# Performance work log

Hardware: AMD Instinct MI355X
Metric: run time of the kernel (lower is better)

Reference implementation:

```python
import jax, jax.numpy as jnp
import numpy as np

B, N, D = 4, 2048, 512   # batch, seq, query_dim
H, DH = 8, 64            # heads, dim_head; inner = H*DH = 512
INNER = H * DH


def setup_inputs() -> dict:
    key = jax.random.key(0)
    ks = jax.random.split(key, 5)
    s = 1.0 / np.sqrt(D)
    return {
        "x": jax.random.normal(ks[0], (B, N, D), dtype=jnp.float32),
        "mask": jnp.ones((B, N), dtype=bool),
        "Wq": jax.random.uniform(ks[1], (D, INNER), jnp.float32, -s, s),
        "Wkv": jax.random.uniform(ks[2], (D, 2 * INNER), jnp.float32, -s, s),
        "Wout": jax.random.uniform(ks[3], (INNER, D), jnp.float32, -s, s),
        "bout": jax.random.uniform(ks[4], (D,), jnp.float32, -s, s),
    }


def reference(x, mask, Wq, Wkv, Wout, bout):
    scale = DH ** -0.5
    q = x @ Wq                                   # [B, N, H*DH]
    kv = x @ Wkv                                 # context defaults to x (self-attn)
    k, v = jnp.split(kv, 2, axis=-1)
    # b n (h d) -> b h n d
    q = q.reshape(B, N, H, DH).transpose(0, 2, 1, 3)
    k = k.reshape(B, N, H, DH).transpose(0, 2, 1, 3)
    v = v.reshape(B, N, H, DH).transpose(0, 2, 1, 3)
    sim = jnp.einsum('bhid,bhjd->bhij', q, k) * scale  # [B, H, N, N]
    max_neg = -jnp.finfo(sim.dtype).max
    sim = jnp.where(mask[:, None, None, :], sim, max_neg)
    attn = jax.nn.softmax(sim, axis=-1)
    out = jnp.einsum('bhij,bhjd->bhid', attn, v)       # [B, H, N, DH]
    out = out.transpose(0, 2, 1, 3).reshape(B, N, INNER)
    return out @ Wout + bout                           # drop_path_rate=0 -> Identity
```

## Files before the change

kernel.cpp:

```cpp
#include <hip/hip_runtime.h>
#include <stdint.h>

typedef __bf16 bf16x8 __attribute__((ext_vector_type(8)));
typedef __bf16 bf16x4 __attribute__((ext_vector_type(4)));
typedef float f32x4 __attribute__((ext_vector_type(4)));
typedef float f32x16 __attribute__((ext_vector_type(16)));
typedef unsigned short u16x8 __attribute__((ext_vector_type(8)));
typedef unsigned short u16x4 __attribute__((ext_vector_type(4)));
typedef unsigned int u32x4 __attribute__((ext_vector_type(4)));

#define MFMA16(a, b, c) __builtin_amdgcn_mfma_f32_16x16x32_bf16((a), (b), (c), 0, 0, 0)
#define MFMA32(a, b, c) __builtin_amdgcn_mfma_f32_32x32x16_bf16((a), (b), (c), 0, 0, 0)
#define EXP2(x) __builtin_amdgcn_exp2f(x)

__device__ __forceinline__ unsigned short f2bf(float f) {
    unsigned int u = __builtin_bit_cast(unsigned int, f);
    return (unsigned short)((u + 0x7fffu + ((u >> 16) & 1u)) >> 16);
}

__device__ __forceinline__ unsigned int cvtpk(float lo, float hi) {
    unsigned int r;
    asm("v_cvt_pk_bf16_f32 %0, %1, %2" : "=v"(r) : "v"(lo), "v"(hi));
    return r;
}

__device__ __forceinline__ void pl32swap(unsigned int& a, unsigned int& b) {
    asm volatile("v_permlane32_swap_b32 %0, %1" : "+v"(a), "+v"(b));
}

__device__ __forceinline__ void gl_lds16(const void* g, void* l) {
    __builtin_amdgcn_global_load_lds(
        (const __attribute__((address_space(1))) unsigned int*)g,
        (__attribute__((address_space(3))) unsigned int*)l, 16, 0, 0);
}

#define BTOK   8192
#define DMODEL 512
#define NQKV   1536
#define SEQ    2048
#define NH     8
#define DH     64
#define QSCL   0.18033688011112043f

__global__ __launch_bounds__(256) void prep_kernel(
    const float* __restrict__ x, const float* __restrict__ Wq,
    const float* __restrict__ Wkv, const float* __restrict__ Wout,
    unsigned short* __restrict__ xb, unsigned short* __restrict__ wqkv_t,
    unsigned short* __restrict__ wout_t)
{
    int64_t idx = (int64_t)blockIdx.x * blockDim.x + threadIdx.x;
    const int64_t NXV = (int64_t)BTOK * DMODEL / 8;
    const int64_t NW1 = (int64_t)NQKV * DMODEL;
    const int64_t NW2 = (int64_t)DMODEL * DMODEL;
    if (idx < NXV) {
        const float* s = x + idx * 8;
        u16x8 o8;
#pragma unroll
        for (int j = 0; j < 8; ++j) o8[j] = f2bf(s[j]);
        *(u16x8*)&xb[idx * 8] = o8;
        return;
    }
    idx -= NXV;
    if (idx < NW1) {
        int o = (int)(idx >> 9), i = (int)(idx & 511);
        float v = (o < 512) ? Wq[i * 512 + o] : Wkv[i * 1024 + (o - 512)];
        wqkv_t[idx] = f2bf(v);
        return;
    }
    idx -= NW1;
    if (idx < NW2) {
        int o = (int)(idx >> 9), i = (int)(idx & 511);
        wout_t[idx] = f2bf(Wout[i * 512 + o]);
    }
}

template <int BF16_OUT, int QSCALE>
__global__ __launch_bounds__(256) void gemm_bt(
    const unsigned short* __restrict__ A, const unsigned short* __restrict__ Bt,
    void* __restrict__ Cout, const float* __restrict__ bias,
    int M, int N, int K)
{
    __shared__ __align__(16) unsigned short As[128 * 32];
    __shared__ __align__(16) unsigned short Bs[128 * 32];
    const int tid = threadIdx.x;
    const int lid = tid & 63, w = tid >> 6;
    const int wr = w >> 1, wc = w & 1;
    const int l16 = lid & 15, lg = lid >> 4;
    const int m0 = blockIdx.x * 128, n0 = blockIdx.y * 128;

    f32x4 acc[4][4] = {};

    for (int k0 = 0; k0 < K; k0 += 32) {
#pragma unroll
        for (int s = 0; s < 2; ++s) {
            int chunk = s * 256 + w * 64 + lid;
            int r = chunk >> 2, off = (chunk & 3) * 8;
            gl_lds16(&A[(int64_t)(m0 + r) * K + k0 + off], &As[(s * 256 + w * 64) * 8]);
            gl_lds16(&Bt[(int64_t)(n0 + r) * K + k0 + off], &Bs[(s * 256 + w * 64) * 8]);
        }
        __syncthreads();
        bf16x8 af[4], bfr[4];
#pragma unroll
        for (int i = 0; i < 4; ++i) {
            af[i]  = *(const bf16x8*)&As[(wr * 64 + i * 16 + l16) * 32 + lg * 8];
            bfr[i] = *(const bf16x8*)&Bs[(wc * 64 + i * 16 + l16) * 32 + lg * 8];
        }
#pragma unroll
        for (int i = 0; i < 4; ++i)
#pragma unroll
            for (int j = 0; j < 4; ++j)
                acc[i][j] = MFMA16(af[i], bfr[j], acc[i][j]);
        __syncthreads();
    }

#pragma unroll
    for (int i = 0; i < 4; ++i) {
        int row = m0 + wr * 64 + i * 16 + lg * 4;
#pragma unroll
        for (int j = 0; j < 4; ++j) {
            int col = n0 + wc * 64 + j * 16 + l16;
#pragma unroll
            for (int e = 0; e < 4; ++e) {
                float v = acc[i][j][e];
                if (QSCALE && col < 512) v *= QSCL;
                if (BF16_OUT) {
                    ((unsigned short*)Cout)[(int64_t)(row + e) * N + col] = f2bf(v);
                } else {
                    ((float*)Cout)[(int64_t)(row + e) * N + col] = v + bias[col];
                }
            }
        }
    }
}

__global__ __launch_bounds__(256, 4) void attn_kernel(
    const unsigned short* __restrict__ qkv, unsigned short* __restrict__ attn_out)
{
    __shared__ __align__(16) char smem[32768];

    const int tid = threadIdx.x;
    const int lid = tid & 63, w = tid >> 6;
    const int qg = w & 1, half = w >> 1;
    const int tid128 = tid & 127;
    const int l31 = lid & 31, g = lid >> 5;

    const int bid = blockIdx.y * 32 + blockIdx.x;
    const int nb = (bid & 7) * 128 + (bid >> 3);
    const int bx = nb & 31, bh = nb >> 5;
    const int b = bh >> 3, h = bh & 7;

    const int64_t rowbase = (int64_t)b * SEQ;
    const unsigned short* qp = qkv + rowbase * NQKV + h * DH;
    const unsigned short* kp = qp + 512;
    const unsigned short* vp = qp + 1024;
    const int qrow = bx * 64 + qg * 32 + l31;

    unsigned short* Hb = (unsigned short*)smem + half * 8192;

    int kro[2], kso[2];
#pragma unroll
    for (int s = 0; s < 2; ++s) {
        int chunk = s * 128 + tid128;
        int r = chunk >> 3, cc = chunk & 7;
        int key = (r ^ (r >> 3)) & 7;
        kro[s] = r; kso[s] = (cc ^ key) * 8;
    }
    const int t4 = tid128 >> 4, d4 = tid128 & 15;
    const int c2wb = t4 >> 2;
    const int kvlo = (2 * t4) & 7;
    int dpart[4];
#pragma unroll
    for (int u = 0; u < 4; ++u)
        dpart[u] = (d4 * 4 + u) * 64 + kvlo * 2;

    const int kk = (l31 ^ (l31 >> 3)) & 7;
    const int kd = ((l31 >> 2) ^ l31) & 3;

    bf16x8 qf[4];
#pragma unroll
    for (int ks = 0; ks < 4; ++ks)
        qf[ks] = *(const bf16x8*)&qp[(int64_t)qrow * NQKV + ks * 16 + g * 8];

    f32x16 ot0 = {}, ot1 = {};
    float ssum = 0.f;
    u16x4 pv[4];

#define STAGE_K(T, BUF) {                                                     \
    const unsigned short* kpt_ = kp + (int64_t)(T) * 32 * NQKV;               \
    unsigned short* kb_ = Hb + (BUF) * 2048;                                  \
    _Pragma("unroll")                                                         \
    for (int s_ = 0; s_ < 2; ++s_)                                            \
        gl_lds16(&kpt_[(int64_t)kro[s_] * NQKV + kso[s_]],                    \
                 &kb_[s_ * 1024 + qg * 512]); }

#define LOAD_V(T) {                                                           \
    const unsigned short* vpt_ = vp + (int64_t)(T) * 32 * NQKV;               \
    _Pragma("unroll")                                                         \
    for (int s_ = 0; s_ < 2; ++s_) {                                          \
        int row_ = s_ * 16 + 2 * t4;                                          \
        pv[s_ * 2]     = *(const u16x4*)&vpt_[(int64_t)row_ * NQKV + d4 * 4];         \
        pv[s_ * 2 + 1] = *(const u16x4*)&vpt_[(int64_t)(row_ + 1) * NQKV + d4 * 4]; } }

#define WRITE_V(BUF) {                                                        \
    char* vb_ = (char*)(Hb + 4096 + (BUF) * 2048);                            \
    _Pragma("unroll")                                                         \
    for (int s_ = 0; s_ < 2; ++s_) {                                          \
        int c2w_ = 2 * s_ + c2wb;                                             \
        _Pragma("unroll")                                                     \
        for (int u_ = 0; u_ < 4; ++u_) {                                      \
            int kdw_ = (d4 & 3) ^ u_;                                         \
            int off_ = dpart[u_] + (((c2w_ ^ kdw_) & 3) * 16);                \
            *(unsigned int*)(vb_ + off_) =                                    \
                (unsigned int)pv[s_ * 2][u_] |                                \
                ((unsigned int)pv[s_ * 2 + 1][u_] << 16);                     \
        } } }

    const int tb = half * 32;
    LOAD_V(tb + 0);
    WRITE_V(0);
    LOAD_V(tb + 1);
    WRITE_V(1);
    STAGE_K(tb + 0, 0);
    __syncthreads();

    const int NT = 32;
    for (int t = 0; t < NT; ++t) {
        const int bc = t & 1, bn = bc ^ 1;
        const bool p1 = (t + 1 < NT), p2 = (t + 2 < NT);

        if (p1) STAGE_K(tb + t + 1, bn);
        if (p2) LOAD_V(tb + t + 2);

        f32x16 st = {};
        {
            const unsigned short* kb = Hb + bc * 2048;
            __builtin_amdgcn_s_setprio(1);
#pragma unroll
            for (int ks = 0; ks < 4; ++ks) {
                int c8 = (ks * 2 + g) ^ kk;
                bf16x8 ka = *(const bf16x8*)&kb[l31 * 64 + c8 * 8];
                st = MFMA32(ka, qf[ks], st);
            }
            __builtin_amdgcn_s_setprio(0);
        }

#pragma unroll
        for (int r = 0; r < 16; ++r) st[r] = EXP2(st[r]);
        float p0 = (st[0] + st[1]) + (st[2] + st[3]);
        float p1v = (st[4] + st[5]) + (st[6] + st[7]);
        float p2v = (st[8] + st[9]) + (st[10] + st[11]);
        float p3v = (st[12] + st[13]) + (st[14] + st[15]);
        ssum += (p0 + p1v) + (p2v + p3v);

        bf16x8 pf[2];
#define PFRAG(HALFI, OUT) {                                               \
        unsigned int a0 = cvtpk(st[8 * HALFI + 0], st[8 * HALFI + 1]);    \
        unsigned int a1 = cvtpk(st[8 * HALFI + 2], st[8 * HALFI + 3]);    \
        unsigned int b0 = cvtpk(st[8 * HALFI + 4], st[8 * HALFI + 5]);    \
        unsigned int b1 = cvtpk(st[8 * HALFI + 6], st[8 * HALFI + 7]);    \
        pl32swap(a0, b0); pl32swap(a1, b1);                               \
        u32x4 t_ = {a0, a1, b0, b1};                                      \
        OUT = __builtin_bit_cast(bf16x8, t_); }
        PFRAG(0, pf[0]); PFRAG(1, pf[1]);
#undef PFRAG

        {
            const unsigned short* vb = Hb + 4096 + bc * 2048;
            __builtin_amdgcn_s_setprio(1);
#pragma unroll
            for (int kstep = 0; kstep < 2; ++kstep) {
                int c2 = (kstep * 2 + g) ^ kd;
                bf16x8 va0 = *(const bf16x8*)&vb[l31 * 32 + c2 * 8];
                bf16x8 va1 = *(const bf16x8*)&vb[(32 + l31) * 32 + c2 * 8];
                ot0 = MFMA32(va0, pf[kstep], ot0);
                ot1 = MFMA32(va1, pf[kstep], ot1);
            }
            __builtin_amdgcn_s_setprio(0);
        }

        if (p1) __syncthreads();
        if (p2) WRITE_V(bc);
    }
#undef STAGE_K
#undef LOAD_V
#undef WRITE_V

    ssum += __shfl_xor(ssum, 32);

    __syncthreads();
    float* Ob  = (float*)smem;
    float* Ssb = (float*)(smem + 16896);
    if (half) {
        float* dst = Ob + (qg * 64 + lid) * 33;
#pragma unroll
        for (int r = 0; r < 16; ++r) { dst[r] = ot0[r]; dst[16 + r] = ot1[r]; }
        Ssb[qg * 64 + lid] = ssum;
    }
    __syncthreads();
    if (!half) {
        const float* src = Ob + (qg * 64 + lid) * 33;
        float inv = 1.0f / (ssum + Ssb[qg * 64 + lid]);
        unsigned short* op = attn_out + (rowbase + qrow) * 512 + h * DH;
#pragma unroll
        for (int rr = 0; rr < 4; ++rr) {
            int d0 = 8 * rr + 4 * g;
            bf16x4 o0, o1;
#pragma unroll
            for (int e = 0; e < 4; ++e) {
                o0[e] = (__bf16)((ot0[rr * 4 + e] + src[rr * 4 + e]) * inv);
                o1[e] = (__bf16)((ot1[rr * 4 + e] + src[16 + rr * 4 + e]) * inv);
            }
            *(bf16x4*)&op[d0] = o0;
            *(bf16x4*)&op[32 + d0] = o1;
        }
    }
}

extern "C" void kernel_launch(void* const* d_in, const int* in_sizes, int n_in,
                              void* d_out, int out_size, void* d_ws, size_t ws_size,
                              hipStream_t stream)
{
    const float* x    = (const float*)d_in[0];
    const float* Wq   = (const float*)d_in[2];
    const float* Wkv  = (const float*)d_in[3];
    const float* Wout = (const float*)d_in[4];
    const float* bout = (const float*)d_in[5];
    float* out = (float*)d_out;

    char* ws = (char*)d_ws;
    unsigned short* xb     = (unsigned short*)(ws);
    unsigned short* wqkv_t = (unsigned short*)(ws + 8388608);
    unsigned short* wout_t = (unsigned short*)(ws + 8388608 + 1572864);
    unsigned short* qkvb   = (unsigned short*)(ws + 10485760);
    unsigned short* attn_o = (unsigned short*)(ws + 35651584);

    prep_kernel<<<6144, 256, 0, stream>>>(x, Wq, Wkv, Wout, xb, wqkv_t, wout_t);

    dim3 g1(64, 12);
    gemm_bt<1, 1><<<g1, 256, 0, stream>>>(xb, wqkv_t, (void*)qkvb, nullptr,
                                          BTOK, NQKV, DMODEL);

    dim3 ga(32, 32);
    attn_kernel<<<ga, 256, 0, stream>>>(qkvb, attn_o);

    dim3 g2(64, 4);
    gemm_bt<0, 0><<<g2, 256, 0, stream>>>(attn_o, wout_t, (void*)out, bout,
                                          BTOK, DMODEL, DMODEL);
}
```

Baseline: 105.2 us.

## Write V transposed from QKV GEMM and stage K/V via direct LDS loads

The QKV projection GEMM now writes V in a per-head transposed [b,h,d,n] layout and Q/K into a separate buffer with stride 1024. The attention kernel can then stage both K and V tiles with global_load_lds directly into a fragment-friendly LDS layout. This removes the register round-trip and the swizzled LDS transpose writes for V. The cost is strided 4-element scattered stores in the GEMM epilogue for V, and the LDS reads are no longer swizzled, which may introduce bank conflicts.

```diff
diff --git a/kernel.cpp b/kernel.cpp
--- a/kernel.cpp
+++ b/kernel.cpp
@@ -37,6 +37,7 @@
 #define BTOK   8192
 #define DMODEL 512
 #define NQKV   1536
+#define QKSTR  1024
 #define SEQ    2048
 #define NH     8
 #define DH     64
@@ -74,11 +75,11 @@
     }
 }
 
-template <int BF16_OUT, int QSCALE>
+template <int BF16_OUT, int QSCALE, int VSPLIT>
 __global__ __launch_bounds__(256) void gemm_bt(
     const unsigned short* __restrict__ A, const unsigned short* __restrict__ Bt,
     void* __restrict__ Cout, const float* __restrict__ bias,
-    int M, int N, int K)
+    unsigned short* __restrict__ vT, int M, int N, int K)
 {
     __shared__ __align__(16) unsigned short As[128 * 32];
     __shared__ __align__(16) unsigned short Bs[128 * 32];
@@ -119,14 +120,24 @@
 #pragma unroll
         for (int j = 0; j < 4; ++j) {
             int col = n0 + wc * 64 + j * 16 + l16;
-#pragma unroll
-            for (int e = 0; e < 4; ++e) {
-                float v = acc[i][j][e];
-                if (QSCALE && col < 512) v *= QSCL;
-                if (BF16_OUT) {
-                    ((unsigned short*)Cout)[(int64_t)(row + e) * N + col] = f2bf(v);
-                } else {
-                    ((float*)Cout)[(int64_t)(row + e) * N + col] = v + bias[col];
+            if (VSPLIT && col >= 1024) {
+                int h = (col - 1024) >> 6, d = (col - 1024) & 63;
+                int b = row >> 11, n = row & 2047;
+                u16x4 o4;
+#pragma unroll
+                for (int e = 0; e < 4; ++e) o4[e] = f2bf(acc[i][j][e]);
+                *(u16x4*)&vT[(((int64_t)(b * 8 + h) * 64 + d) << 11) + n] = o4;
+            } else {
+#pragma unroll
+                for (int e = 0; e < 4; ++e) {
+                    float v = acc[i][j][e];
+                    if (QSCALE && col < 512) v *= QSCL;
+                    if (BF16_OUT) {
+                        int ldc = VSPLIT ? QKSTR : N;
+                        ((unsigned short*)Cout)[(int64_t)(row + e) * ldc + col] = f2bf(v);
+                    } else {
+                        ((float*)Cout)[(int64_t)(row + e) * N + col] = v + bias[col];
+                    }
                 }
             }
         }
@@ -134,14 +145,14 @@
 }
 
 __global__ __launch_bounds__(256, 4) void attn_kernel(
-    const unsigned short* __restrict__ qkv, unsigned short* __restrict__ attn_out)
+    const unsigned short* __restrict__ qk, const unsigned short* __restrict__ vT,
+    unsigned short* __restrict__ attn_out)
 {
     __shared__ __align__(16) char smem[32768];
 
     const int tid = threadIdx.x;
     const int lid = tid & 63, w = tid >> 6;
     const int qg = w & 1, half = w >> 1;
-    const int tid128 = tid & 127;
     const int l31 = lid & 31, g = lid >> 5;
 
     const int bid = blockIdx.y * 32 + blockIdx.x;
@@ -150,86 +161,55 @@
     const int b = bh >> 3, h = bh & 7;
 
     const int64_t rowbase = (int64_t)b * SEQ;
-    const unsigned short* qp = qkv + rowbase * NQKV + h * DH;
+    const unsigned short* qp = qk + rowbase * QKSTR + h * DH;
     const unsigned short* kp = qp + 512;
-    const unsigned short* vp = qp + 1024;
+    const unsigned short* vTp = vT + ((int64_t)bh << 17);
     const int qrow = bx * 64 + qg * 32 + l31;
 
     unsigned short* Hb = (unsigned short*)smem + half * 8192;
 
-    int kro[2], kso[2];
+    int koff[2], vgoff[2];
 #pragma unroll
     for (int s = 0; s < 2; ++s) {
-        int chunk = s * 128 + tid128;
-        int r = chunk >> 3, cc = chunk & 7;
-        int key = (r ^ (r >> 3)) & 7;
-        kro[s] = r; kso[s] = (cc ^ key) * 8;
-    }
-    const int t4 = tid128 >> 4, d4 = tid128 & 15;
-    const int c2wb = t4 >> 2;
-    const int kvlo = (2 * t4) & 7;
-    int dpart[4];
-#pragma unroll
-    for (int u = 0; u < 4; ++u)
-        dpart[u] = (d4 * 4 + u) * 64 + kvlo * 2;
-
-    const int kk = (l31 ^ (l31 >> 3)) & 7;
-    const int kd = ((l31 >> 2) ^ l31) & 3;
+        int rK = lid >> 1, cK = (s * 2 + qg) * 2 + (lid & 1);
+        koff[s] = rK * QKSTR + cK * 8;
+        int dV = qg * 32 + (lid >> 1), c2 = s * 2 + (lid & 1);
+        vgoff[s] = dV * 2048 + c2 * 8;
+    }
 
     bf16x8 qf[4];
 #pragma unroll
     for (int ks = 0; ks < 4; ++ks)
-        qf[ks] = *(const bf16x8*)&qp[(int64_t)qrow * NQKV + ks * 16 + g * 8];
+        qf[ks] = *(const bf16x8*)&qp[(int64_t)qrow * QKSTR + ks * 16 + g * 8];
 
     f32x16 ot0 = {}, ot1 = {};
     float ssum = 0.f;
-    u16x4 pv[4];
 
 #define STAGE_K(T, BUF) {                                                     \
-    const unsigned short* kpt_ = kp + (int64_t)(T) * 32 * NQKV;               \
+    const unsigned short* kpt_ = kp + (int64_t)(T) * 32 * QKSTR;              \
     unsigned short* kb_ = Hb + (BUF) * 2048;                                  \
     _Pragma("unroll")                                                         \
     for (int s_ = 0; s_ < 2; ++s_)                                            \
-        gl_lds16(&kpt_[(int64_t)kro[s_] * NQKV + kso[s_]],                    \
-                 &kb_[s_ * 1024 + qg * 512]); }
-
-#define LOAD_V(T) {                                                           \
-    const unsigned short* vpt_ = vp + (int64_t)(T) * 32 * NQKV;               \
+        gl_lds16(&kpt_[koff[s_]], &kb_[s_ * 1024 + qg * 512]); }
+
+#define STAGE_V(T, BUF) {                                                     \
+    const unsigned short* vpt_ = vTp + (T) * 32;                              \
+    unsigned short* vb_ = Hb + 4096 + (BUF) * 2048;                           \
     _Pragma("unroll")                                                         \
-    for (int s_ = 0; s_ < 2; ++s_) {                                          \
-        int row_ = s_ * 16 + 2 * t4;                                          \
-        pv[s_ * 2]     = *(const u16x4*)&vpt_[(int64_t)row_ * NQKV + d4 * 4];         \
-        pv[s_ * 2 + 1] = *(const u16x4*)&vpt_[(int64_t)(row_ + 1) * NQKV + d4 * 4]; } }
-
-#define WRITE_V(BUF) {                                                        \
-    char* vb_ = (char*)(Hb + 4096 + (BUF) * 2048);                            \
-    _Pragma("unroll")                                                         \
-    for (int s_ = 0; s_ < 2; ++s_) {                                          \
-        int c2w_ = 2 * s_ + c2wb;                                             \
-        _Pragma("unroll")                                                     \
-        for (int u_ = 0; u_ < 4; ++u_) {                                      \
-            int kdw_ = (d4 & 3) ^ u_;                                         \
-            int off_ = dpart[u_] + (((c2w_ ^ kdw_) & 3) * 16);                \
-            *(unsigned int*)(vb_ + off_) =                                    \
-                (unsigned int)pv[s_ * 2][u_] |                                \
-                ((unsigned int)pv[s_ * 2 + 1][u_] << 16);                     \
-        } } }
+    for (int s_ = 0; s_ < 2; ++s_)                                            \
+        gl_lds16(&vpt_[vgoff[s_]], &vb_[s_ * 1024 + qg * 512]); }
 
     const int tb = half * 32;
-    LOAD_V(tb + 0);
-    WRITE_V(0);
-    LOAD_V(tb + 1);
-    WRITE_V(1);
     STAGE_K(tb + 0, 0);
+    STAGE_V(tb + 0, 0);
     __syncthreads();
 
     const int NT = 32;
     for (int t = 0; t < NT; ++t) {
         const int bc = t & 1, bn = bc ^ 1;
-        const bool p1 = (t + 1 < NT), p2 = (t + 2 < NT);
-
-        if (p1) STAGE_K(tb + t + 1, bn);
-        if (p2) LOAD_V(tb + t + 2);
+        const bool p1 = (t + 1 < NT);
+
+        if (p1) { STAGE_K(tb + t + 1, bn); STAGE_V(tb + t + 1, bn); }
 
         f32x16 st = {};
         {
@@ -237,8 +217,7 @@
             __builtin_amdgcn_s_setprio(1);
 #pragma unroll
             for (int ks = 0; ks < 4; ++ks) {
-                int c8 = (ks * 2 + g) ^ kk;
-                bf16x8 ka = *(const bf16x8*)&kb[l31 * 64 + c8 * 8];
+                bf16x8 ka = *(const bf16x8*)&kb[ks * 512 + l31 * 16 + g * 8];
                 st = MFMA32(ka, qf[ks], st);
             }
             __builtin_amdgcn_s_setprio(0);
@@ -269,9 +248,8 @@
             __builtin_amdgcn_s_setprio(1);
 #pragma unroll
             for (int kstep = 0; kstep < 2; ++kstep) {
-                int c2 = (kstep * 2 + g) ^ kd;
-                bf16x8 va0 = *(const bf16x8*)&vb[l31 * 32 + c2 * 8];
-                bf16x8 va1 = *(const bf16x8*)&vb[(32 + l31) * 32 + c2 * 8];
+                bf16x8 va0 = *(const bf16x8*)&vb[kstep * 1024 + l31 * 16 + g * 8];
+                bf16x8 va1 = *(const bf16x8*)&vb[kstep * 1024 + 512 + l31 * 16 + g * 8];
                 ot0 = MFMA32(va0, pf[kstep], ot0);
                 ot1 = MFMA32(va1, pf[kstep], ot1);
             }
@@ -279,11 +257,9 @@
         }
 
         if (p1) __syncthreads();
-        if (p2) WRITE_V(bc);
     }
 #undef STAGE_K
-#undef LOAD_V
-#undef WRITE_V
+#undef STAGE_V
 
     ssum += __shfl_xor(ssum, 32);
 
@@ -330,20 +306,21 @@
     char* ws = (char*)d_ws;
     unsigned short* xb     = (unsigned short*)(ws);
     unsigned short* wqkv_t = (unsigned short*)(ws + 8388608);
-    unsigned short* wout_t = (unsigned short*)(ws + 8388608 + 1572864);
-    unsigned short* qkvb   = (unsigned short*)(ws + 10485760);
-    unsigned short* attn_o = (unsigned short*)(ws + 35651584);
+    unsigned short* wout_t = (unsigned short*)(ws + 9961472);
+    unsigned short* qkb    = (unsigned short*)(ws + 10485760);
+    unsigned short* attn_o = (unsigned short*)(ws + 27262976);
+    unsigned short* vT     = (unsigned short*)(ws + 35651584);
 
     prep_kernel<<<6144, 256, 0, stream>>>(x, Wq, Wkv, Wout, xb, wqkv_t, wout_t);
 
     dim3 g1(64, 12);
-    gemm_bt<1, 1><<<g1, 256, 0, stream>>>(xb, wqkv_t, (void*)qkvb, nullptr,
-                                          BTOK, NQKV, DMODEL);
+    gemm_bt<1, 1, 1><<<g1, 256, 0, stream>>>(xb, wqkv_t, (void*)qkb, nullptr,
+                                             vT, BTOK, NQKV, DMODEL);
 
     dim3 ga(32, 32);
-    attn_kernel<<<ga, 256, 0, stream>>>(qkvb, attn_o);
+    attn_kernel<<<ga, 256, 0, stream>>>(qkb, vT, attn_o);
 
     dim3 g2(64, 4);
-    gemm_bt<0, 0><<<g2, 256, 0, stream>>>(attn_o, wout_t, (void*)out, bout,
-                                          BTOK, DMODEL, DMODEL);
-}
+    gemm_bt<0, 0, 0><<<g2, 256, 0, stream>>>(attn_o, wout_t, (void*)out, bout,
+                                             nullptr, BTOK, DMODEL, DMODEL);
+}
```

New measurement: 105.7 us. No clear change (+0.5%).
